# Kernel optimization log

Hardware: AMD Instinct MI355X
Metric: run time of the kernel (lower is better)

## Reference

```python
import jax, jax.numpy as jnp
import numpy as np

N, D_IN, D, C, TOPK = 8192, 1024, 512, 2, 6
SCALE = D ** -0.5
LN_EPS = 1e-5


def setup_inputs() -> dict:
    key = jax.random.key(0)
    ks = jax.random.split(key, 20)
    s = 0.02
    p = {
        'x': jax.random.normal(ks[0], (N, D_IN), jnp.float32),
        'fc1_w': jax.random.normal(ks[1], (D_IN, D)) * s,
        'fc1_b': jnp.zeros((D,)),
        'wh_w': jax.random.normal(ks[2], (D, D)) * s,
        'wh_b': jnp.zeros((D,)),
        'wt_w': jax.random.normal(ks[3], (D, D)) * s,
        'wt_b': jnp.zeros((D,)),
        'lin1_w': jax.random.normal(ks[4], (D, D)) * s,
        'lin1_b': jnp.zeros((D,)),
        'lin2_w': jax.random.normal(ks[5], (D, D)) * s,
        'lin2_b': jnp.zeros((D,)),
        'att1_w': jax.random.normal(ks[6], (D, D // 2)) * s,
        'att1_b': jnp.zeros((D // 2,)),
        'att2_w': jax.random.normal(ks[7], (D // 2, 1)) * s,
        'att2_b': jnp.zeros((1,)),
        'ln_g': jnp.ones((D,)),
        'ln_b': jnp.zeros((D,)),
        'fc_w': jax.random.normal(ks[8], (D, C)) * s,
        'fc_b': jnp.zeros((C,)),
    }
    return p


def reference(x, fc1_w, fc1_b, wh_w, wh_b, wt_w, wt_b, lin1_w, lin1_b,
              lin2_w, lin2_b, att1_w, att1_b, att2_w, att2_b, ln_g, ln_b,
              fc_w, fc_b):
    # _fc1: Linear + ReLU (dropout = eval identity)
    h = jax.nn.relu(x @ fc1_w + fc1_b)                      # [N, D]
    h = (h + h.mean(axis=0, keepdims=True)) * 0.5
    e_h = h @ wh_w + wh_b                                   # [N, D]
    e_t = h @ wt_w + wt_b                                   # [N, D]
    # dense N x N attention logits, then top-k neighbors
    logits = (e_h * SCALE) @ e_t.T                          # [N, N]
    tw, ti = jax.lax.top_k(logits, TOPK)                    # [N, K]
    Nb_h = e_t[ti]                                          # [N, K, D] gather
    p = jax.nn.softmax(tw, axis=-1)                         # [N, K]
    # eh_r = p * Nb_h + (1 - p) * e_h  (the matmul in torch is a broadcast)
    eh_r = p[..., None] * Nb_h + (1.0 - p)[..., None] * e_h[:, None, :]
    gate = jnp.tanh(e_h[:, None, :] + eh_r)                 # [N, K, D]
    ka = jnp.einsum('nkd,nkd->nk', Nb_h, gate)              # [N, K]
    kp = jax.nn.softmax(ka, axis=-1)                        # [N, K]
    e_Nh = jnp.einsum('nk,nkd->nd', kp, Nb_h)               # [N, D]
    sum_e = jax.nn.leaky_relu((e_h + e_Nh) @ lin1_w + lin1_b)
    bi_e = jax.nn.leaky_relu((e_h * e_Nh) @ lin2_w + lin2_b)
    emb = sum_e + bi_e                                      # [N, D]
    # GlobalAttention readout over all N nodes (batch=None -> one graph)
    att = jax.nn.leaky_relu(emb @ att1_w + att1_b) @ att2_w + att2_b  # [N,1]
    a = jax.nn.softmax(att, axis=0)                         # [N, 1]
    pooled = jnp.sum(a * emb, axis=0, keepdims=True)        # [1, D]
    # LayerNorm
    mu = pooled.mean(axis=-1, keepdims=True)
    var = pooled.var(axis=-1, keepdims=True)
    ln = (pooled - mu) * jax.lax.rsqrt(var + LN_EPS) * ln_g + ln_b
    out = ln @ fc_w + fc_b                                  # [1, C]
    Y_prob = jax.nn.softmax(out, axis=-1)
    Y_hat = jnp.argmax(out, axis=-1, keepdims=True)
    return out, Y_prob, Y_hat
```

## Files before the change

### kernel.cpp

```cpp
#include <hip/hip_runtime.h>
#include <hip/hip_bf16.h>
#include <cstdint>
#include <math.h>

typedef unsigned short u16;
typedef unsigned int u32;
typedef __bf16 bh;
typedef bh bh8 __attribute__((ext_vector_type(8)));
typedef float f32x4 __attribute__((ext_vector_type(4)));

#define SCALE_F 0.04419417382415922f

__device__ __forceinline__ float bf2f(u16 u) {
    union { float f; unsigned int i; } v; v.i = ((unsigned int)u) << 16; return v.f;
}
__device__ __forceinline__ u16 f2bf(float f) {
    __hip_bfloat16 h = __float2bfloat16(f);
    return __builtin_bit_cast(u16, h);
}
__device__ __forceinline__ bh8 ld8_f32(const float* p) {
    float4 f0 = *(const float4*)p;
    float4 f1 = *(const float4*)(p + 4);
    bh8 r;
    r[0] = (bh)f0.x; r[1] = (bh)f0.y; r[2] = (bh)f0.z; r[3] = (bh)f0.w;
    r[4] = (bh)f1.x; r[5] = (bh)f1.y; r[6] = (bh)f1.z; r[7] = (bh)f1.w;
    return r;
}

__device__ __forceinline__ u32 ordf(float f) {
    u32 u = __float_as_uint(f);
    return u ^ ((u32)((int)u >> 31) | 0x80000000u);
}
__device__ __forceinline__ float unordf(u32 s) {
    u32 u = (s & 0x80000000u) ? (s ^ 0x80000000u) : ~s;
    return __uint_as_float(u);
}
__device__ __forceinline__ u32 pack_vi(float v, int inv_idx) {
    return (ordf(v) & 0xFFFFFF00u) | (u32)inv_idx;
}
__device__ __forceinline__ float unpack_v(u32 p) {
    return unordf(p & 0xFFFFFF00u);
}

__device__ __forceinline__ void gl_lds16(const u16* g, u16* l) {
    __builtin_amdgcn_global_load_lds(
        (const __attribute__((address_space(1))) void*)g,
        (__attribute__((address_space(3))) void*)l, 16, 0, 0);
}

__device__ __forceinline__ void xcd_swz(int bid, int& x, int& y) {
    int xcd = bid & 7, idx = bid >> 3;
    x = idx >> 3;
    y = xcd * 8 + (idx & 7);
}

__global__ void transpose_cvt(const float* s0, u16* d0, const float* s1, u16* d1,
                              const float* s2, u16* d2, const float* s3, u16* d3,
                              const float* s4, u16* d4, const float* s5, u16* d5,
                              const float* xs, u16* xd) {
    int b = blockIdx.x;
    if (b >= 1664) {
        int t = threadIdx.y * 32 + threadIdx.x;
        size_t i = ((size_t)(b - 1664) * 256 + t) * 8;
        *(bh8*)(xd + i) = ld8_f32(xs + i);
        return;
    }
    __shared__ float tsh[32][33];
    const float* src; u16* dst; int R, C, tt;
    if      (b < 512)  { src = s0; dst = d0; R = 1024; C = 512; tt = b; }
    else if (b < 768)  { src = s1; dst = d1; R = 512;  C = 512; tt = b - 512; }
    else if (b < 1024) { src = s2; dst = d2; R = 512;  C = 512; tt = b - 768; }
    else if (b < 1280) { src = s3; dst = d3; R = 512;  C = 512; tt = b - 1024; }
    else if (b < 1536) { src = s4; dst = d4; R = 512;  C = 512; tt = b - 1280; }
    else               { src = s5; dst = d5; R = 512;  C = 256; tt = b - 1536; }
    int ntx = C >> 5;
    int bx = (tt % ntx) * 32, by = (tt / ntx) * 32;
    int x = threadIdx.x, y = threadIdx.y;
    for (int i = 0; i < 32; i += 8)
        tsh[y + i][x] = src[(size_t)(by + y + i) * C + bx + x];
    __syncthreads();
    for (int i = 0; i < 32; i += 8)
        dst[(size_t)(bx + y + i) * R + by + x] = f2bf(tsh[x][y + i]);
}

template<int KT, int NF>
__device__ __forceinline__ void kloop64(const u16* __restrict__ Ag, const u16* __restrict__ Bg,
                                        u16* Alds, u16* Blds, f32x4 (&acc)[2][NF]) {
    const int tid = threadIdx.x;
    const int wave = tid >> 6, lane = tid & 63;
    const int lr = lane & 15, quad = lane >> 4;
    const int wm = (wave & 1) * 32, wn = (wave >> 1) * (NF * 16);
    const int r = tid >> 2;
    const int g8 = (((tid & 3) ^ ((tid >> 3) & 3))) * 8;
    const int kbr8 = (quad ^ ((lr >> 1) & 3)) * 8;
    const u16* ga  = Ag + (size_t)r * KT + g8;
    const u16* gb0 = Bg + (size_t)r * KT + g8;
    const u16* gb1 = gb0 + (size_t)64 * KT;
    u16* la = Alds + wave * 512;
    u16* lb = Blds + wave * 512;
    #pragma unroll
    for (int k0 = 0; k0 < KT; k0 += 32) {
        __syncthreads();
        gl_lds16(ga + k0, la);
        gl_lds16(gb0 + k0, lb);
        if (NF == 4) gl_lds16(gb1 + k0, lb + 2048);
        __syncthreads();
        bh8 af[2], bf_[NF];
        #pragma unroll
        for (int i = 0; i < 2; i++)
            af[i] = *(const bh8*)&Alds[(wm + i * 16 + lr) * 32 + kbr8];
        #pragma unroll
        for (int i = 0; i < NF; i++)
            bf_[i] = *(const bh8*)&Blds[(wn + i * 16 + lr) * 32 + kbr8];
        #pragma unroll
        for (int mi = 0; mi < 2; mi++)
            #pragma unroll
            for (int ni = 0; ni < NF; ni++)
                acc[mi][ni] = __builtin_amdgcn_mfma_f32_16x16x32_bf16(
                    af[mi], bf_[ni], acc[mi][ni], 0, 0, 0);
    }
}

template<int ACT, int F32OUT>
__device__ __forceinline__ void epilogue64(f32x4 (&acc)[2][2], const float* bias,
                                           float* Cf, u16* Cb, int N, int m0, int n0) {
    const int tid = threadIdx.x;
    const int wave = tid >> 6, lane = tid & 63;
    const int lr = lane & 15, quad = lane >> 4;
    const int wm = (wave & 1) * 32, wn = (wave >> 1) * 32;
    #pragma unroll
    for (int ni = 0; ni < 2; ni++) {
        int col = n0 + wn + ni * 16 + lr;
        float bs = bias[col];
        #pragma unroll
        for (int mi = 0; mi < 2; mi++) {
            #pragma unroll
            for (int i = 0; i < 4; i++) {
                int row = m0 + wm + mi * 16 + quad * 4 + i;
                float v = acc[mi][ni][i] + bs;
                if (ACT == 1) v = fmaxf(v, 0.0f);
                if (ACT == 2) v = (v > 0.0f) ? v : 0.01f * v;
                size_t o = (size_t)row * N + col;
                if (F32OUT) Cf[o] = v;
                else        Cb[o] = f2bf(v);
            }
        }
    }
}

template<int ACT, int F32OUT, int KT>
__global__ __launch_bounds__(256) void gemm64(
    const u16* __restrict__ A, const u16* __restrict__ B, const float* __restrict__ bias,
    float* __restrict__ Cf, u16* __restrict__ Cb, int N)
{
    __shared__ __align__(16) u16 Alds[64 * 32];
    __shared__ __align__(16) u16 Blds[64 * 32];
    const int m0 = blockIdx.y * 64, n0 = blockIdx.x * 64;
    f32x4 acc[2][2] = {};
    kloop64<KT, 2>(A + (size_t)m0 * KT, B + (size_t)n0 * KT, Alds, Blds, acc);
    epilogue64<ACT, F32OUT>(acc, bias, Cf, Cb, N, m0, n0);
}

template<int KT>
__device__ __forceinline__ void kloop128p(const u16* __restrict__ Ag,
                                          const u16* __restrict__ Bg,
                                          u16* lds, f32x4 (&acc)[4][4]) {
    const int tid = threadIdx.x;
    const int wave = tid >> 6, lane = tid & 63;
    const int lr = lane & 15, quad = lane >> 4;
    const int wm = (wave & 1) * 64, wn = (wave >> 1) * 64;
    const int r = tid >> 2;
    const int g8 = (((tid & 3) ^ ((tid >> 3) & 3))) * 8;
    const int kbr8 = (quad ^ ((lr >> 1) & 3)) * 8;
    const u16* ga0 = Ag + (size_t)r * KT + g8;
    const u16* ga1 = ga0 + (size_t)64 * KT;
    const u16* gb0 = Bg + (size_t)r * KT + g8;
    const u16* gb1 = gb0 + (size_t)64 * KT;
    const int wofs = wave * 512;
    constexpr int NT = KT / 32;
    gl_lds16(ga0,      lds + wofs);
    gl_lds16(ga1,      lds + wofs + 2048);
    gl_lds16(gb0,      lds + 4096 + wofs);
    gl_lds16(gb1,      lds + 4096 + wofs + 2048);
    gl_lds16(ga0 + 32, lds + 8192 + wofs);
    gl_lds16(ga1 + 32, lds + 8192 + wofs + 2048);
    gl_lds16(gb0 + 32, lds + 8192 + 4096 + wofs);
    gl_lds16(gb1 + 32, lds + 8192 + 4096 + wofs + 2048);
    #pragma unroll
    for (int t = 0; t < NT; t++) {
        if (t + 1 < NT) asm volatile("s_waitcnt vmcnt(4)" ::: "memory");
        else            asm volatile("s_waitcnt vmcnt(0)" ::: "memory");
        __builtin_amdgcn_s_barrier();
        if (t + 2 < NT) {
            const int k2 = (t + 2) * 32;
            u16* b = lds + ((t + 2) % 3) * 8192;
            gl_lds16(ga0 + k2, b + wofs);
            gl_lds16(ga1 + k2, b + wofs + 2048);
            gl_lds16(gb0 + k2, b + 4096 + wofs);
            gl_lds16(gb1 + k2, b + 4096 + wofs + 2048);
        }
        const u16* Ab = lds + (t % 3) * 8192;
        const u16* Bb = Ab + 4096;
        bh8 af[4], bf_[4];
        #pragma unroll
        for (int i = 0; i < 4; i++) {
            af[i]  = *(const bh8*)&Ab[(wm + i * 16 + lr) * 32 + kbr8];
            bf_[i] = *(const bh8*)&Bb[(wn + i * 16 + lr) * 32 + kbr8];
        }
        __builtin_amdgcn_s_setprio(1);
        #pragma unroll
        for (int mi = 0; mi < 4; mi++)
            #pragma unroll
            for (int ni = 0; ni < 4; ni++)
                acc[mi][ni] = __builtin_amdgcn_mfma_f32_16x16x32_bf16(
                    af[mi], bf_[ni], acc[mi][ni], 0, 0, 0);
        __builtin_amdgcn_s_setprio(0);
    }
}

template<int ACT, int F32OUT>
__device__ __forceinline__ void epilogue128(f32x4 (&acc)[4][4], const float* bias,
                                            float* Cf, u16* Cb, int N, int m0, int n0) {
    const int tid = threadIdx.x;
    const int wave = tid >> 6, lane = tid & 63;
    const int lr = lane & 15, quad = lane >> 4;
    const int wm = (wave & 1) * 64, wn = (wave >> 1) * 64;
    #pragma unroll
    for (int ni = 0; ni < 4; ni++) {
        int col = n0 + wn + ni * 16 + lr;
        float bs = bias[col];
        #pragma unroll
        for (int mi = 0; mi < 4; mi++) {
            #pragma unroll
            for (int i = 0; i < 4; i++) {
                int row = m0 + wm + mi * 16 + quad * 4 + i;
                float v = acc[mi][ni][i] + bs;
                if (ACT == 1) v = fmaxf(v, 0.0f);
                if (ACT == 2) v = (v > 0.0f) ? v : 0.01f * v;
                size_t o = (size_t)row * N + col;
                if (F32OUT) Cf[o] = v;
                else        Cb[o] = f2bf(v);
            }
        }
    }
}

template<int ACT, int F32OUT, int KT, int GNX>
__global__ __launch_bounds__(256) void gemm128(
    const u16* __restrict__ A, const u16* __restrict__ B, const float* __restrict__ bias,
    float* __restrict__ Cf, u16* __restrict__ Cb, int N)
{
    __shared__ __align__(16) u16 ldsbuf[3 * 8192];
    int bx, by;
    xcd_swz(blockIdx.y * GNX + blockIdx.x, bx, by);
    const int m0 = by * 128, n0 = bx * 128;
    f32x4 acc[4][4] = {};
    kloop128p<KT>(A + (size_t)m0 * KT, B + (size_t)n0 * KT, ldsbuf, acc);
    epilogue128<ACT, F32OUT>(acc, bias, Cf, Cb, N, m0, n0);
}

__global__ __launch_bounds__(256) void ehet128(
    const u16* __restrict__ A, const u16* __restrict__ Bh, const u16* __restrict__ Bt,
    const float* __restrict__ bh_, const float* __restrict__ bt_,
    u16* __restrict__ Oh, u16* __restrict__ Ot)
{
    __shared__ __align__(16) u16 ldsbuf[3 * 8192];
    int bx, by;
    xcd_swz(blockIdx.y * 8 + blockIdx.x, bx, by);
    const int m0 = by * 128, n0 = (bx & 3) * 128;
    const u16* B = (bx < 4) ? Bh : Bt;
    const float* bias = (bx < 4) ? bh_ : bt_;
    u16* O = (bx < 4) ? Oh : Ot;
    f32x4 acc[4][4] = {};
    kloop128p<512>(A + (size_t)m0 * 512, B + (size_t)n0 * 512, ldsbuf, acc);
    epilogue128<0, 0>(acc, bias, nullptr, O, 512, m0, n0);
}

__global__ __launch_bounds__(256) void lin12_128(
    const u16* __restrict__ A1, const u16* __restrict__ B1, const float* __restrict__ b1,
    const u16* __restrict__ A2, const u16* __restrict__ B2, const float* __restrict__ b2,
    u16* __restrict__ O)
{
    __shared__ __align__(16) u16 ldsbuf[3 * 8192];
    int bx, by;
    xcd_swz(blockIdx.y * 4 + blockIdx.x, bx, by);
    const int m0 = by * 128, n0 = bx * 128;
    f32x4 acc1[4][4] = {}, acc2[4][4] = {};
    kloop128p<512>(A1 + (size_t)m0 * 512, B1 + (size_t)n0 * 512, ldsbuf, acc1);
    __syncthreads();
    kloop128p<512>(A2 + (size_t)m0 * 512, B2 + (size_t)n0 * 512, ldsbuf, acc2);
    const int tid = threadIdx.x;
    const int wave = tid >> 6, lane = tid & 63;
    const int lr = lane & 15, quad = lane >> 4;
    const int wm = (wave & 1) * 64, wn = (wave >> 1) * 64;
    #pragma unroll
    for (int ni = 0; ni < 4; ni++) {
        int col = n0 + wn + ni * 16 + lr;
        float bs1 = b1[col], bs2 = b2[col];
        #pragma unroll
        for (int mi = 0; mi < 4; mi++) {
            #pragma unroll
            for (int i = 0; i < 4; i++) {
                int row = m0 + wm + mi * 16 + quad * 4 + i;
                float v1 = acc1[mi][ni][i] + bs1;
                v1 = (v1 > 0.0f) ? v1 : 0.01f * v1;
                float v2 = acc2[mi][ni][i] + bs2;
                v2 = (v2 > 0.0f) ? v2 : 0.01f * v2;
                O[(size_t)row * 512 + col] = f2bf(v1 + v2);
            }
        }
    }
}

template<int KT>
__device__ __forceinline__ void kloop256w(const u16* __restrict__ Ag,
                                          const u16* __restrict__ Bg,
                                          u16* lds, f32x4 (&acc)[4][8]) {
    const int tid = threadIdx.x;
    const int wave = tid >> 6, lane = tid & 63;
    const int lr = lane & 15, quad = lane >> 4;
    const int wm = (wave & 1) * 64;
    const int r = tid >> 2;
    const int g8 = (((tid & 3) ^ ((tid >> 3) & 3))) * 8;
    const int kbr8 = (quad ^ ((lr >> 1) & 3)) * 8;
    const u16* ga0 = Ag + (size_t)r * KT + g8;
    const u16* ga1 = ga0 + (size_t)64 * KT;
    const u16* gb0 = Bg + (size_t)r * KT + g8;
    const u16* gb1 = gb0 + (size_t)64 * KT;
    const u16* gb2 = gb0 + (size_t)128 * KT;
    const u16* gb3 = gb0 + (size_t)192 * KT;
    const int wofs = wave * 512;
    constexpr int NT = KT / 32;
    constexpr int BUF = 12288;
    auto stage = [&](int t, int koff) {
        u16* b = lds + (t % 3) * BUF;
        gl_lds16(ga0 + koff, b + wofs);
        gl_lds16(ga1 + koff, b + wofs + 2048);
        gl_lds16(gb0 + koff, b + 4096 + wofs);
        gl_lds16(gb1 + koff, b + 4096 + wofs + 2048);
        gl_lds16(gb2 + koff, b + 8192 + wofs);
        gl_lds16(gb3 + koff, b + 8192 + wofs + 2048);
    };
    stage(0, 0);
    stage(1, 32);
    #pragma unroll
    for (int t = 0; t < NT; t++) {
        if (t + 1 < NT) asm volatile("s_waitcnt vmcnt(6)" ::: "memory");
        else            asm volatile("s_waitcnt vmcnt(0)" ::: "memory");
        __builtin_amdgcn_s_barrier();
        if (t + 2 < NT) stage(t + 2, (t + 2) * 32);
        const u16* Ab = lds + (t % 3) * BUF;
        const u16* Bb = Ab + 4096 + (wave >> 1) * 4096;
        bh8 af[4];
        #pragma unroll
        for (int i = 0; i < 4; i++)
            af[i] = *(const bh8*)&Ab[(wm + i * 16 + lr) * 32 + kbr8];
        __builtin_amdgcn_s_setprio(1);
        #pragma unroll
        for (int g = 0; g < 2; g++) {
            bh8 bf_[4];
            #pragma unroll
            for (int j = 0; j < 4; j++)
                bf_[j] = *(const bh8*)&Bb[((g * 4 + j) * 16 + lr) * 32 + kbr8];
            #pragma unroll
            for (int mi = 0; mi < 4; mi++)
                #pragma unroll
                for (int j = 0; j < 4; j++)
                    acc[mi][g * 4 + j] = __builtin_amdgcn_mfma_f32_16x16x32_bf16(
                        af[mi], bf_[j], acc[mi][g * 4 + j], 0, 0, 0);
        }
        __builtin_amdgcn_s_setprio(0);
    }
}

__global__ __launch_bounds__(256, 2) void logits_topk(
    const u16* __restrict__ Ah, const u16* __restrict__ Bt, u32* __restrict__ tvp)
{
    __shared__ __align__(16) u16 ldsbuf[3 * 12288];
    u32* S = (u32*)ldsbuf;
    const int tid = threadIdx.x;
    int bx, by;
    xcd_swz(blockIdx.y * 32 + blockIdx.x, bx, by);
    const int m0 = by * 128;
    const int cb0 = bx * 256;
    const int lane = tid & 63, wave = tid >> 6;
    const int wh = wave & 1;
    const int wnh = wave >> 1;
    const int lr = lane & 15, quad = lane >> 4;
    const int srow = tid >> 2, scg = tid & 3;

    f32x4 acc[4][8] = {};
    kloop256w<512>(Ah + (size_t)m0 * 512, Bt + (size_t)cb0 * 512, ldsbuf, acc);

    u32 v[2][6] = {{0,0,0,0,0,0},{0,0,0,0,0,0}};
    #pragma unroll
    for (int h = 0; h < 2; h++) {
        #pragma unroll
        for (int nh = 0; nh < 2; nh++) {
            __syncthreads();
            if (wh == h && wnh == nh) {
                #pragma unroll
                for (int mi = 0; mi < 4; mi++)
                    #pragma unroll
                    for (int f = 0; f < 8; f++)
                        #pragma unroll
                        for (int i = 0; i < 4; i++) {
                            int colLocal = nh * 128 + f * 16 + lr;
                            S[(mi * 16 + quad * 4 + i) * 129 + f * 16 + lr]
                                = pack_vi(acc[mi][f][i], 255 - colLocal);
                        }
            }
            __syncthreads();
            const u32* Sr = &S[srow * 129 + scg * 8];
            #pragma unroll
            for (int ch = 0; ch < 4; ch++) {
                #pragma unroll
                for (int c = 0; c < 8; c++) {
                    u32 x = Sr[ch * 32 + c];
                    v[h][5] = max(v[h][5], min(v[h][4], x));
                    v[h][4] = max(v[h][4], min(v[h][3], x));
                    v[h][3] = max(v[h][3], min(v[h][2], x));
                    v[h][2] = max(v[h][2], min(v[h][1], x));
                    v[h][1] = max(v[h][1], min(v[h][0], x));
                    v[h][0] = max(v[h][0], x);
                }
            }
        }
    }
    #pragma unroll
    for (int h = 0; h < 2; h++) {
        __syncthreads();
        {
            u32* dst = &S[srow * 129 + scg * 6];
            #pragma unroll
            for (int j = 0; j < 6; j++) dst[j] = v[h][j];
        }
        __syncthreads();
        if (tid < 64) {
            u32 m0v = 0, m1v = 0, m2v = 0, m3v = 0, m4v = 0, m5v = 0;
            const u32* Sr = &S[tid * 129];
            #pragma unroll
            for (int s = 0; s < 24; s++) {
                u32 x = Sr[s];
                m5v = max(m5v, min(m4v, x));
                m4v = max(m4v, min(m3v, x));
                m3v = max(m3v, min(m2v, x));
                m2v = max(m2v, min(m1v, x));
                m1v = max(m1v, min(m0v, x));
                m0v = max(m0v, x);
            }
            u32* dst = tvp + (size_t)(m0 + h * 64 + tid) * 192 + bx * 6;
            dst[0] = m0v; dst[1] = m1v; dst[2] = m2v;
            dst[3] = m3v; dst[4] = m4v; dst[5] = m5v;
        }
    }
}

__global__ void topk_merge(const u32* __restrict__ tvp,
                           float* __restrict__ tv, int* __restrict__ ti)
{
    int r = blockIdx.x * 64 + threadIdx.x;
    u32 v[6]; int ix[6];
    #pragma unroll
    for (int j = 0; j < 6; j++) { v[j] = 0; ix[j] = 0; }
    const u32* pv = tvp + (size_t)r * 192;
    for (int b = 0; b < 32; b++) {
        #pragma unroll
        for (int j2 = 0; j2 < 6; j2++) {
            u32 p = pv[b * 6 + j2];
            if (p <= v[5]) break;
            v[5] = p; ix[5] = b * 256 + 255 - (int)(p & 255u);
            #pragma unroll
            for (int j = 5; j > 0; j--) {
                if (v[j] > v[j - 1]) {
                    u32 tf = v[j]; v[j] = v[j - 1]; v[j - 1] = tf;
                    int tx = ix[j]; ix[j] = ix[j - 1]; ix[j - 1] = tx;
                }
            }
        }
    }
    #pragma unroll
    for (int j = 0; j < 6; j++) {
        tv[(size_t)r * 6 + j] = unpack_v(v[j]) * SCALE_F;
        ti[(size_t)r * 6 + j] = ix[j];
    }
}

__global__ __launch_bounds__(256) void neighbor_kernel(
    const u16* __restrict__ eH, const u16* __restrict__ eT,
    const float* __restrict__ tv, const int* __restrict__ ti,
    u16* __restrict__ s1, u16* __restrict__ s2)
{
    const int tid = threadIdx.x, wave = tid >> 6, lane = tid & 63;
    const int n = blockIdx.x * 4 + wave;
    float tw[6]; int id[6];
    #pragma unroll
    for (int j = 0; j < 6; j++) {
        tw[j] = tv[n * 6 + j];
        int t = ti[n * 6 + j];
        id[j] = ((unsigned)t < 8192u) ? t : 0;
    }
    float mx = tw[0];
    #pragma unroll
    for (int j = 1; j < 6; j++) mx = fmaxf(mx, tw[j]);
    float p[6]; float ps = 0.f;
    #pragma unroll
    for (int j = 0; j < 6; j++) { p[j] = __expf(tw[j] - mx); ps += p[j]; }
    float inv = 1.0f / ps;
    #pragma unroll
    for (int j = 0; j < 6; j++) p[j] *= inv;

    const size_t base = (size_t)n * 512 + lane * 8;
    float eh[8];
    { bh8 v = *(const bh8*)(eH + base);
      #pragma unroll
      for (int c = 0; c < 8; c++) eh[c] = (float)v[c]; }
    float nb[6][8];
    #pragma unroll
    for (int j = 0; j < 6; j++) {
        bh8 v = *(const bh8*)(eT + (size_t)id[j] * 512 + lane * 8);
        #pragma unroll
        for (int c = 0; c < 8; c++) nb[j][c] = (float)v[c];
    }
    float ka[6];
    #pragma unroll
    for (int j = 0; j < 6; j++) {
        float s = 0.f;
        #pragma unroll
        for (int c = 0; c < 8; c++) {
            float e = p[j] * nb[j][c] + (1.f - p[j]) * eh[c];
            float x = eh[c] + e;
            x = fminf(fmaxf(x, -15.f), 15.f);
            float ex = __expf(2.f * x);
            float g = 1.f - 2.f / (ex + 1.f);
            s += nb[j][c] * g;
        }
        #pragma unroll
        for (int off = 32; off > 0; off >>= 1) s += __shfl_down(s, off);
        ka[j] = __shfl(s, 0);
    }
    float m2 = ka[0];
    #pragma unroll
    for (int j = 1; j < 6; j++) m2 = fmaxf(m2, ka[j]);
    float kp[6]; float ks = 0.f;
    #pragma unroll
    for (int j = 0; j < 6; j++) { kp[j] = __expf(ka[j] - m2); ks += kp[j]; }
    float inv2 = 1.0f / ks;
    #pragma unroll
    for (int j = 0; j < 6; j++) kp[j] *= inv2;
    bh8 o1, o2;
    #pragma unroll
    for (int c = 0; c < 8; c++) {
        float eN = 0.f;
        #pragma unroll
        for (int j = 0; j < 6; j++) eN += kp[j] * nb[j][c];
        o1[c] = (bh)(eh[c] + eN);
        o2[c] = (bh)(eh[c] * eN);
    }
    *(bh8*)(s1 + base) = o1;
    *(bh8*)(s2 + base) = o2;
}

__global__ void colsum_kernel(const u16* __restrict__ h, float* __restrict__ colsum) {
    int tid = threadIdx.x;
    int n0 = blockIdx.x * 32;
    float a0 = 0.f, a1 = 0.f;
    for (int k = 0; k < 32; k++) {
        size_t b = (size_t)(n0 + k) * 512;
        a0 += bf2f(h[b + tid]); a1 += bf2f(h[b + tid + 256]);
    }
    atomicAdd(&colsum[tid], a0);
    atomicAdd(&colsum[tid + 256], a1);
}

__global__ void meanmix_kernel(u16* __restrict__ h, const float* __restrict__ colsum) {
    size_t i = ((size_t)blockIdx.x * 256 + threadIdx.x) * 8;
    int col = (int)(i & 511);
    union { int4 v; u16 s[8]; } u;
    u.v = *(const int4*)&h[i];
    #pragma unroll
    for (int j = 0; j < 8; j++)
        u.s[j] = f2bf((bf2f(u.s[j]) + colsum[col + j] * (1.0f / 8192.0f)) * 0.5f);
    *(int4*)&h[i] = u.v;
}

__global__ __launch_bounds__(256) void att2_kernel(
    const float* __restrict__ a1, const float* __restrict__ w,
    const float* __restrict__ b, float* __restrict__ att)
{
    int row = blockIdx.x * 4 + (threadIdx.x >> 6);
    int lane = threadIdx.x & 63;
    const float* pr = a1 + (size_t)row * 256;
    float s = 0.f;
    #pragma unroll
    for (int k = 0; k < 4; k++) { int c = lane + k * 64; s += pr[c] * w[c]; }
    #pragma unroll
    for (int off = 32; off > 0; off >>= 1) s += __shfl_down(s, off);
    if (lane == 0) att[row] = s + b[0];
}

__global__ void att_max(const float* __restrict__ att, u32* __restrict__ scal_u) {
    int i = blockIdx.x * 256 + threadIdx.x;
    int lane = threadIdx.x & 63;
    u32 o = ordf(att[i]);
    #pragma unroll
    for (int off = 32; off > 0; off >>= 1) o = max(o, (u32)__shfl_down((int)o, off));
    if (lane == 0) atomicMax(&scal_u[0], o);
}
__global__ void att_sum(const float* __restrict__ att, float* __restrict__ scal) {
    int i = blockIdx.x * 256 + threadIdx.x;
    int lane = threadIdx.x & 63;
    float mx = unordf(((const u32*)scal)[0]);
    float e = __expf(att[i] - mx);
    #pragma unroll
    for (int off = 32; off > 0; off >>= 1) e += __shfl_down(e, off);
    if (lane == 0) atomicAdd(&scal[1], e);
}

__global__ void pooled_kernel(const u16* __restrict__ emb, const float* __restrict__ att,
                              const float* __restrict__ scal, float* __restrict__ pooled) {
    int tid = threadIdx.x;
    int n0 = blockIdx.x * 32;
    float mx = unordf(((const u32*)scal)[0]);
    float inv = 1.0f / scal[1];
    float a0 = 0.f, a1 = 0.f;
    for (int k = 0; k < 32; k++) {
        int n = n0 + k;
        float w = __expf(att[n] - mx) * inv;
        size_t b = (size_t)n * 512;
        a0 += w * bf2f(emb[b + tid]);
        a1 += w * bf2f(emb[b + tid + 256]);
    }
    atomicAdd(&pooled[tid], a0);
    atomicAdd(&pooled[tid + 256], a1);
}

__global__ void final_kernel(const float* __restrict__ pooled,
                             const float* __restrict__ g, const float* __restrict__ bln,
                             const float* __restrict__ fcw, const float* __restrict__ fcb,
                             float* __restrict__ out) {
    __shared__ float red[256];
    int tid = threadIdx.x;
    float x0 = pooled[tid], x1 = pooled[tid + 256];
    red[tid] = x0 + x1; __syncthreads();
    for (int s = 128; s > 0; s >>= 1) { if (tid < s) red[tid] += red[tid + s]; __syncthreads(); }
    float mu = red[0] * (1.0f / 512.0f); __syncthreads();
    float d0 = x0 - mu, d1 = x1 - mu;
    red[tid] = d0 * d0 + d1 * d1; __syncthreads();
    for (int s = 128; s > 0; s >>= 1) { if (tid < s) red[tid] += red[tid + s]; __syncthreads(); }
    float var = red[0] * (1.0f / 512.0f); __syncthreads();
    float rstd = rsqrtf(var + 1e-5f);
    float l0 = d0 * rstd * g[tid]       + bln[tid];
    float l1 = d1 * rstd * g[tid + 256] + bln[tid + 256];
    red[tid] = l0 * fcw[tid * 2] + l1 * fcw[(tid + 256) * 2]; __syncthreads();
    for (int s = 128; s > 0; s >>= 1) { if (tid < s) red[tid] += red[tid + s]; __syncthreads(); }
    float o0 = red[0] + fcb[0]; __syncthreads();
    red[tid] = l0 * fcw[tid * 2 + 1] + l1 * fcw[(tid + 256) * 2 + 1]; __syncthreads();
    for (int s = 128; s > 0; s >>= 1) { if (tid < s) red[tid] += red[tid + s]; __syncthreads(); }
    float o1 = red[0] + fcb[1];
    if (tid == 0) {
        float m = fmaxf(o0, o1);
        float e0 = expf(o0 - m), e1 = expf(o1 - m);
        float se = e0 + e1;
        out[0] = o0;
        out[1] = o1;
        out[2] = e0 / se;
        out[3] = e1 / se;
        out[4] = (o0 >= o1) ? 0.0f : 1.0f;
    }
}

extern "C" void kernel_launch(void* const* d_in, const int* in_sizes, int n_in,
                              void* d_out, int out_size, void* d_ws, size_t ws_size,
                              hipStream_t stream)
{
    const float* x      = (const float*)d_in[0];
    const float* fc1_w  = (const float*)d_in[1];
    const float* fc1_b  = (const float*)d_in[2];
    const float* wh_w   = (const float*)d_in[3];
    const float* wh_b   = (const float*)d_in[4];
    const float* wt_w   = (const float*)d_in[5];
    const float* wt_b   = (const float*)d_in[6];
    const float* lin1_w = (const float*)d_in[7];
    const float* lin1_b = (const float*)d_in[8];
    const float* lin2_w = (const float*)d_in[9];
    const float* lin2_b = (const float*)d_in[10];
    const float* att1_w = (const float*)d_in[11];
    const float* att1_b = (const float*)d_in[12];
    const float* att2_w = (const float*)d_in[13];
    const float* att2_b = (const float*)d_in[14];
    const float* ln_g   = (const float*)d_in[15];
    const float* ln_b   = (const float*)d_in[16];
    const float* fc_w   = (const float*)d_in[17];
    const float* fc_b   = (const float*)d_in[18];
    float* out = (float*)d_out;
    char* ws = (char*)d_ws;

    u16*   fc1T   = (u16*)(ws + 0);
    u16*   whT    = (u16*)(ws + 1048576);
    u16*   wtT    = (u16*)(ws + 1572864);
    u16*   l1T    = (u16*)(ws + 2097152);
    u16*   l2T    = (u16*)(ws + 2621440);
    u16*   a1T    = (u16*)(ws + 3145728);
    float* tv     = (float*)(ws + 3407872);
    int*   ti     = (int*)(ws + 3604480);
    float* att    = (float*)(ws + 3801088);
    float* colsum = (float*)(ws + 3833856);
    float* pooled = (float*)(ws + 3835904);
    float* scal   = (float*)(ws + 3837952);
    u32*   tvp    = (u32*)(ws + 4194304);
    u16*   hbf    = (u16*)(ws + 14680064);
    u16*   ehbf   = (u16*)(ws + 23068672);
    u16*   etbf   = (u16*)(ws + 31457280);
    u16*   s2bf   = (u16*)(ws + 39845888);
    u16*   xbf    = (u16*)(ws + 23068672);
    float* a1f    = (float*)(ws + 23068672);

    transpose_cvt<<<5760, dim3(32, 8), 0, stream>>>(
        fc1_w, fc1T, wh_w, whT, wt_w, wtT, lin1_w, l1T, lin2_w, l2T, att1_w, a1T, x, xbf);
    hipMemsetAsync(colsum, 0, 4160, stream);

    gemm128<1, 0, 1024, 4><<<dim3(4, 64), 256, 0, stream>>>(xbf, fc1T, fc1_b, nullptr, hbf, 512);
    colsum_kernel<<<256, 256, 0, stream>>>(hbf, colsum);
    meanmix_kernel<<<2048, 256, 0, stream>>>(hbf, colsum);

    ehet128<<<dim3(8, 64), 256, 0, stream>>>(hbf, whT, wtT, wh_b, wt_b, ehbf, etbf);

    logits_topk<<<dim3(32, 64), 256, 0, stream>>>(ehbf, etbf, tvp);
    topk_merge<<<128, 64, 0, stream>>>(tvp, tv, ti);

    neighbor_kernel<<<2048, 256, 0, stream>>>(ehbf, etbf, tv, ti, hbf, s2bf);

    lin12_128<<<dim3(4, 64), 256, 0, stream>>>(hbf, l1T, lin1_b, s2bf, l2T, lin2_b, etbf);

    gemm64<2, 1, 512><<<dim3(4, 128), 256, 0, stream>>>(etbf, a1T, att1_b, a1f, nullptr, 256);
    att2_kernel<<<2048, 256, 0, stream>>>(a1f, att2_w, att2_b, att);
    att_max<<<32, 256, 0, stream>>>(att, (u32*)scal);
    att_sum<<<32, 256, 0, stream>>>(att, scal);
    pooled_kernel<<<256, 256, 0, stream>>>(etbf, att, scal, pooled);

    final_kernel<<<1, 256, 0, stream>>>(pooled, ln_g, ln_b, fc_w, fc_b, out);
}
```

Baseline: 342.3 us.

## Split logits_topk tile across eight waves with 64x64 per-wave subtiles

The fused logits+top-k kernel now launches 512 threads per block instead of 256. Each wave computes a 64x64 sub-tile instead of 64x128, so the per-wave accumulator array is halved. Global-to-LDS staging is spread over twice as many threads, and the top-k reduction epilogue is re-indexed to 8 column groups of 16 with a 48-entry final merge. The aim is more waves in flight and lower register pressure to hide memory and LDS latency, at the cost of more LDS fragment reads per MFMA and more work on the shared reduction.

```diff
diff --git a/kernel.cpp b/kernel.cpp
--- a/kernel.cpp
+++ b/kernel.cpp
@@ -313,67 +313,57 @@
 }
 
 template<int KT>
-__device__ __forceinline__ void kloop256w(const u16* __restrict__ Ag,
-                                          const u16* __restrict__ Bg,
-                                          u16* lds, f32x4 (&acc)[4][8]) {
+__device__ __forceinline__ void kloop256w8(const u16* __restrict__ Ag,
+                                           const u16* __restrict__ Bg,
+                                           u16* lds, f32x4 (&acc)[4][4]) {
     const int tid = threadIdx.x;
     const int wave = tid >> 6, lane = tid & 63;
     const int lr = lane & 15, quad = lane >> 4;
     const int wm = (wave & 1) * 64;
+    const int wq = wave >> 1;
     const int r = tid >> 2;
     const int g8 = (((tid & 3) ^ ((tid >> 3) & 3))) * 8;
     const int kbr8 = (quad ^ ((lr >> 1) & 3)) * 8;
-    const u16* ga0 = Ag + (size_t)r * KT + g8;
-    const u16* ga1 = ga0 + (size_t)64 * KT;
+    const u16* ga  = Ag + (size_t)r * KT + g8;
     const u16* gb0 = Bg + (size_t)r * KT + g8;
-    const u16* gb1 = gb0 + (size_t)64 * KT;
-    const u16* gb2 = gb0 + (size_t)128 * KT;
-    const u16* gb3 = gb0 + (size_t)192 * KT;
+    const u16* gb1 = gb0 + (size_t)128 * KT;
     const int wofs = wave * 512;
     constexpr int NT = KT / 32;
     constexpr int BUF = 12288;
     auto stage = [&](int t, int koff) {
         u16* b = lds + (t % 3) * BUF;
-        gl_lds16(ga0 + koff, b + wofs);
-        gl_lds16(ga1 + koff, b + wofs + 2048);
+        gl_lds16(ga  + koff, b + wofs);
         gl_lds16(gb0 + koff, b + 4096 + wofs);
-        gl_lds16(gb1 + koff, b + 4096 + wofs + 2048);
-        gl_lds16(gb2 + koff, b + 8192 + wofs);
-        gl_lds16(gb3 + koff, b + 8192 + wofs + 2048);
+        gl_lds16(gb1 + koff, b + 8192 + wofs);
     };
     stage(0, 0);
     stage(1, 32);
     #pragma unroll
     for (int t = 0; t < NT; t++) {
-        if (t + 1 < NT) asm volatile("s_waitcnt vmcnt(6)" ::: "memory");
+        if (t + 1 < NT) asm volatile("s_waitcnt vmcnt(3)" ::: "memory");
         else            asm volatile("s_waitcnt vmcnt(0)" ::: "memory");
         __builtin_amdgcn_s_barrier();
         if (t + 2 < NT) stage(t + 2, (t + 2) * 32);
         const u16* Ab = lds + (t % 3) * BUF;
-        const u16* Bb = Ab + 4096 + (wave >> 1) * 4096;
-        bh8 af[4];
-        #pragma unroll
-        for (int i = 0; i < 4; i++)
-            af[i] = *(const bh8*)&Ab[(wm + i * 16 + lr) * 32 + kbr8];
+        const u16* Bb = Ab + 4096 + wq * 2048;
+        bh8 af[4], bf_[4];
+        #pragma unroll
+        for (int i = 0; i < 4; i++) {
+            af[i]  = *(const bh8*)&Ab[(wm + i * 16 + lr) * 32 + kbr8];
+            bf_[i] = *(const bh8*)&Bb[(i * 16 + lr) * 32 + kbr8];
+        }
         __builtin_amdgcn_s_setprio(1);
         #pragma unroll
-        for (int g = 0; g < 2; g++) {
-            bh8 bf_[4];
-            #pragma unroll
-            for (int j = 0; j < 4; j++)
-                bf_[j] = *(const bh8*)&Bb[((g * 4 + j) * 16 + lr) * 32 + kbr8];
-            #pragma unroll
-            for (int mi = 0; mi < 4; mi++)
-                #pragma unroll
-                for (int j = 0; j < 4; j++)
-                    acc[mi][g * 4 + j] = __builtin_amdgcn_mfma_f32_16x16x32_bf16(
-                        af[mi], bf_[j], acc[mi][g * 4 + j], 0, 0, 0);
-        }
+        for (int mi = 0; mi < 4; mi++)
+            #pragma unroll
+            for (int ni = 0; ni < 4; ni++)
+                acc[mi][ni] = __builtin_amdgcn_mfma_f32_16x16x32_bf16(
+                    af[mi], bf_[ni], acc[mi][ni], 0, 0, 0);
         __builtin_amdgcn_s_setprio(0);
     }
 }
 
-__global__ __launch_bounds__(256, 2) void logits_topk(
+__global__ __launch_bounds__(512, 2) void logits_topk(
     const u16* __restrict__ Ah, const u16* __restrict__ Bt, u32* __restrict__ tvp)
 {
     __shared__ __align__(16) u16 ldsbuf[3 * 12288];
@@ -385,12 +375,12 @@
     const int cb0 = bx * 256;
     const int lane = tid & 63, wave = tid >> 6;
     const int wh = wave & 1;
-    const int wnh = wave >> 1;
+    const int wq = wave >> 1;
     const int lr = lane & 15, quad = lane >> 4;
-    const int srow = tid >> 2, scg = tid & 3;
-
-    f32x4 acc[4][8] = {};
-    kloop256w<512>(Ah + (size_t)m0 * 512, Bt + (size_t)cb0 * 512, ldsbuf, acc);
+    const int srow = tid >> 3, scg = tid & 7;
+
+    f32x4 acc[4][4] = {};
+    kloop256w8<512>(Ah + (size_t)m0 * 512, Bt + (size_t)cb0 * 512, ldsbuf, acc);
 
     u32 v[2][6] = {{0,0,0,0,0,0},{0,0,0,0,0,0}};
     #pragma unroll
@@ -398,32 +388,29 @@
         #pragma unroll
         for (int nh = 0; nh < 2; nh++) {
             __syncthreads();
-            if (wh == h && wnh == nh) {
+            if (wh == h && (wq >> 1) == nh) {
                 #pragma unroll
                 for (int mi = 0; mi < 4; mi++)
                     #pragma unroll
-                    for (int f = 0; f < 8; f++)
+                    for (int ni = 0; ni < 4; ni++)
                         #pragma unroll
                         for (int i = 0; i < 4; i++) {
-                            int colLocal = nh * 128 + f * 16 + lr;
-                            S[(mi * 16 + quad * 4 + i) * 129 + f * 16 + lr]
-                                = pack_vi(acc[mi][f][i], 255 - colLocal);
+                            int colLocal = wq * 64 + ni * 16 + lr;
+                            S[(mi * 16 + quad * 4 + i) * 129 + (colLocal - nh * 128)]
+                                = pack_vi(acc[mi][ni][i], 255 - colLocal);
                         }
             }
             __syncthreads();
-            const u32* Sr = &S[srow * 129 + scg * 8];
-            #pragma unroll
-            for (int ch = 0; ch < 4; ch++) {
-                #pragma unroll
-                for (int c = 0; c < 8; c++) {
-                    u32 x = Sr[ch * 32 + c];
-                    v[h][5] = max(v[h][5], min(v[h][4], x));
-                    v[h][4] = max(v[h][4], min(v[h][3], x));
-                    v[h][3] = max(v[h][3], min(v[h][2], x));
-                    v[h][2] = max(v[h][2], min(v[h][1], x));
-                    v[h][1] = max(v[h][1], min(v[h][0], x));
-                    v[h][0] = max(v[h][0], x);
-                }
+            const u32* Sr = &S[srow * 129 + scg * 16];
+            #pragma unroll
+            for (int c = 0; c < 16; c++) {
+                u32 x = Sr[c];
+                v[h][5] = max(v[h][5], min(v[h][4], x));
+                v[h][4] = max(v[h][4], min(v[h][3], x));
+                v[h][3] = max(v[h][3], min(v[h][2], x));
+                v[h][2] = max(v[h][2], min(v[h][1], x));
+                v[h][1] = max(v[h][1], min(v[h][0], x));
+                v[h][0] = max(v[h][0], x);
             }
         }
     }
@@ -440,7 +427,7 @@
             u32 m0v = 0, m1v = 0, m2v = 0, m3v = 0, m4v = 0, m5v = 0;
             const u32* Sr = &S[tid * 129];
             #pragma unroll
-            for (int s = 0; s < 24; s++) {
+            for (int s = 0; s < 48; s++) {
                 u32 x = Sr[s];
                 m5v = max(m5v, min(m4v, x));
                 m4v = max(m4v, min(m3v, x));
@@ -726,7 +713,7 @@
 
     ehet128<<<dim3(8, 64), 256, 0, stream>>>(hbf, whT, wtT, wh_b, wt_b, ehbf, etbf);
 
-    logits_topk<<<dim3(32, 64), 256, 0, stream>>>(ehbf, etbf, tvp);
+    logits_topk<<<dim3(32, 64), 512, 0, stream>>>(ehbf, etbf, tvp);
     topk_merge<<<128, 64, 0, stream>>>(tvp, tv, ti);
 
     neighbor_kernel<<<2048, 256, 0, stream>>>(ehbf, etbf, tv, ti, hbf, s2bf);
```

Measured after the change: 353.1 us. 3.2% more time.
